# Kernel tuning notes

Measured on AMD Instinct MI355X. Metric: run time of the kernel, lower is better.

## Reference

```python
import jax, jax.numpy as jnp
import numpy as np

N_NODES = 50000
N_EDGES = 800000
N_INC = 64
E_OUTC = 64
HS1 = 128
HS2 = 128
LN_EPS = 1e-5


def setup_inputs() -> dict:
    key = jax.random.key(0)
    ks = jax.random.split(key, 8)
    scale1 = 1.0 / np.sqrt(N_INC + E_OUTC)
    scale2 = 1.0 / np.sqrt(HS1)
    return {
        "x": jax.random.normal(ks[0], (N_NODES, N_INC), dtype=jnp.float32),
        "edge_attr": jax.random.normal(ks[1], (N_EDGES, E_OUTC), dtype=jnp.float32),
        "edge_index": jax.random.randint(ks[2], (2, N_EDGES), 0, N_NODES, dtype=jnp.int64)
        if jax.config.jax_enable_x64 else jax.random.randint(ks[2], (2, N_EDGES), 0, N_NODES, dtype=jnp.int32),
        "W1": jax.random.normal(ks[3], (N_INC + E_OUTC, HS1), dtype=jnp.float32) * scale1,
        "b1": jnp.zeros((HS1,), dtype=jnp.float32),
        "ln_g": jnp.ones((HS1,), dtype=jnp.float32),
        "ln_b": jnp.zeros((HS1,), dtype=jnp.float32),
        "W2": jax.random.normal(ks[4], (HS1, HS2), dtype=jnp.float32) * scale2,
        "b2": jnp.zeros((HS2,), dtype=jnp.float32),
    }


def reference(x, edge_attr, edge_index, W1, b1, ln_g, ln_b, W2, b2):
    # _agg: gather source nodes, concat with edge features -> [E, n_inc+e_outc]
    row, col = edge_index[0], edge_index[1]
    h = jnp.concatenate([x[row], edge_attr], axis=1)
    # node_mlp_1: Linear -> LayerNorm -> ReLU -> Linear
    h = h @ W1 + b1
    mu = jnp.mean(h, axis=-1, keepdims=True)
    var = jnp.mean(jnp.square(h - mu), axis=-1, keepdims=True)
    h = (h - mu) * jax.lax.rsqrt(var + LN_EPS) * ln_g + ln_b
    h = jax.nn.relu(h)
    h = h @ W2 + b2  # [E, HS2]
    # scatter_mean into destination nodes, dim_size = N
    n = x.shape[0]
    sums = jax.ops.segment_sum(h, col, num_segments=n)
    cnt = jax.ops.segment_sum(jnp.ones((h.shape[0],), dtype=h.dtype), col, num_segments=n)
    return sums / jnp.maximum(cnt, 1.0)[:, None]
```

## Files before the change

### kernel.cpp

```cpp
#include <hip/hip_runtime.h>
#include <hip/hip_bf16.h>


typedef __bf16 bf16x8 __attribute__((ext_vector_type(8)));
typedef float f32x4 __attribute__((ext_vector_type(4)));

#define LN_EPS 1e-5f

__device__ __forceinline__ unsigned short bfbits(float f) {
  return __builtin_bit_cast(unsigned short, (__bf16)f);
}
__device__ __forceinline__ float bflo(unsigned int u) { return __uint_as_float(u << 16); }
__device__ __forceinline__ float bfhi(unsigned int u) { return __uint_as_float(u & 0xffff0000u); }
__device__ __forceinline__ unsigned int pkbf(float a, float b) {
  return (unsigned int)bfbits(a) | ((unsigned int)bfbits(b) << 16);
}

__global__ void hist_kernel(const int* __restrict__ eidx, int* __restrict__ cnt, int E) {
  int e = blockIdx.x * blockDim.x + threadIdx.x;
  if (e < E) atomicAdd(&cnt[eidx[E + e]], 1);
}

__global__ void scan_kernel(const int* __restrict__ cnt, int* __restrict__ off, int n) {
  __shared__ int wsum[16];
  __shared__ int carry_s;
  const int tid = threadIdx.x;
  const int wv = tid >> 6;
  const int ln = tid & 63;
  if (tid == 0) carry_s = 0;
  __syncthreads();
  for (int base = 0; base < n; base += 4096) {
    int i0 = base + tid * 4;
    int a = (i0 < n) ? cnt[i0] : 0;
    int b = (i0 + 1 < n) ? cnt[i0 + 1] : 0;
    int c = (i0 + 2 < n) ? cnt[i0 + 2] : 0;
    int d = (i0 + 3 < n) ? cnt[i0 + 3] : 0;
    int lsum = a + b + c + d;
    int sc = lsum;
#pragma unroll
    for (int dl = 1; dl < 64; dl <<= 1) {
      int t = __shfl_up(sc, dl);
      if (ln >= dl) sc += t;
    }
    if (ln == 63) wsum[wv] = sc;
    __syncthreads();
    int woff = 0;
#pragma unroll
    for (int w = 0; w < 16; ++w) {
      int t = wsum[w];
      if (w < wv) woff += t;
    }
    int excl = carry_s + woff + sc - lsum;
    if (i0 < n) off[i0] = excl;
    if (i0 + 1 < n) off[i0 + 1] = excl + a;
    if (i0 + 2 < n) off[i0 + 2] = excl + a + b;
    if (i0 + 3 < n) off[i0 + 3] = excl + a + b + c;
    __syncthreads();
    if (tid == 1023) carry_s = carry_s + woff + sc;
    __syncthreads();
  }
}

__global__ void scatter_kernel(const int* __restrict__ eidx, const int* __restrict__ off,
                               int* __restrict__ cur, int* __restrict__ perm,
                               int* __restrict__ rowp, int E) {
  int e = blockIdx.x * blockDim.x + threadIdx.x;
  if (e < E) {
    int c = eidx[E + e];
    int p = atomicAdd(&cur[c], 1);
    int pos = off[c] + p;
    perm[pos] = e;
    if (rowp) rowp[pos] = eidx[e];
  }
}

template <bool ATOMIC>
__global__ __launch_bounds__(512, 2) void mlp_kernel(
    const float* __restrict__ x, const float* __restrict__ ea,
    const int* __restrict__ eidx, const int* __restrict__ perm,
    const int* __restrict__ rowp, const float* __restrict__ W1,
    const float* __restrict__ b1, const float* __restrict__ lng,
    const float* __restrict__ lnb, const float* __restrict__ W2,
    const float* __restrict__ b2, float* __restrict__ out,
    unsigned short* __restrict__ h2, int E, int ntiles) {
  __shared__ __align__(16) unsigned int w1L[2048 * 4];
  __shared__ __align__(16) unsigned int w2L[2048 * 4];
  __shared__ float b1L[128];
  __shared__ float b2L[128];
  __shared__ unsigned int glcL[128];
  __shared__ __align__(16) char hbuf[8][16 * 272];

  const int tid = threadIdx.x;
  const int lane = tid & 63;
  const int wv = tid >> 6;
  const int e15 = lane & 15;
  const int q = lane >> 4;
  char* hb = hbuf[wv];

  for (int c = tid; c < 2048; c += 512) {
    const int fragid = c >> 6;
    const int l = c & 63;
    const int ks = fragid >> 3, mt = fragid & 7;
    const int qq = l >> 4, ee = l & 15;
    const size_t base = (size_t)(ks * 32 + qq * 8) * 128 + mt * 16 + ee;
    unsigned int p1[4], p2[4];
#pragma unroll
    for (int jj = 0; jj < 4; ++jj) {
      p1[jj] = pkbf(W1[base + (size_t)(2 * jj) * 128], W1[base + (size_t)(2 * jj + 1) * 128]);
      p2[jj] = pkbf(W2[base + (size_t)(2 * jj) * 128], W2[base + (size_t)(2 * jj + 1) * 128]);
    }
    uint4 v1 = {p1[0], p1[1], p1[2], p1[3]};
    uint4 v2 = {p2[0], p2[1], p2[2], p2[3]};
    *(uint4*)&w1L[c * 4] = v1;
    *(uint4*)&w2L[c * 4] = v2;
  }
  if (tid < 128) {
    b1L[tid] = b1[tid];
    b2L[tid] = b2[tid];
    glcL[tid] = pkbf(lng[tid], lnb[tid]);
  }
  __syncthreads();

  const int nwav = (gridDim.x * blockDim.x) >> 6;
  const int wid = (blockIdx.x * blockDim.x + tid) >> 6;

  auto mlp_core = [&](const float4 (&raw)[8], f32x4 (&c2)[8]) {
    bf16x8 bfr[4];
#pragma unroll
    for (int ks = 0; ks < 4; ++ks) {
      const float* p0 = (const float*)&raw[2 * ks];
      const float* p1 = (const float*)&raw[2 * ks + 1];
#pragma unroll
      for (int j = 0; j < 4; ++j) {
        bfr[ks][j] = (__bf16)p0[j];
        bfr[ks][4 + j] = (__bf16)p1[j];
      }
    }
    f32x4 c1[8];
#pragma unroll
    for (int mt = 0; mt < 8; ++mt) {
      float4 bv = *(const float4*)&b1L[mt * 16 + q * 4];
      c1[mt][0] = bv.x;
      c1[mt][1] = bv.y;
      c1[mt][2] = bv.z;
      c1[mt][3] = bv.w;
    }
#pragma unroll
    for (int ks = 0; ks < 4; ++ks)
#pragma unroll
      for (int mt = 0; mt < 8; ++mt) {
        bf16x8 wf = __builtin_bit_cast(
            bf16x8, *(const uint4*)&w1L[((ks * 8 + mt) * 64 + lane) * 4]);
        c1[mt] = __builtin_amdgcn_mfma_f32_16x16x32_bf16(wf, bfr[ks], c1[mt], 0, 0, 0);
      }

    float s = 0.f, ss = 0.f;
#pragma unroll
    for (int mt = 0; mt < 8; ++mt)
#pragma unroll
      for (int r = 0; r < 4; ++r) {
        float v = c1[mt][r];
        s += v;
        ss += v * v;
      }
    s += __shfl_xor(s, 16);
    s += __shfl_xor(s, 32);
    ss += __shfl_xor(ss, 16);
    ss += __shfl_xor(ss, 32);
    const float mu = s * 0.0078125f;
    const float var = ss * 0.0078125f - mu * mu;
    const float inv = rsqrtf(var + LN_EPS);
#pragma unroll
    for (int mt = 0; mt < 8; ++mt) {
      uint4 gv = *(const uint4*)&glcL[mt * 16 + q * 4];
      unsigned int g[4] = {gv.x, gv.y, gv.z, gv.w};
      unsigned short u[4];
#pragma unroll
      for (int r = 0; r < 4; ++r) {
        float v = (c1[mt][r] - mu) * inv;
        v = v * bflo(g[r]) + bfhi(g[r]);
        v = fmaxf(v, 0.f);
        u[r] = bfbits(v);
      }
      uint2 w;
      w.x = (unsigned int)u[0] | ((unsigned int)u[1] << 16);
      w.y = (unsigned int)u[2] | ((unsigned int)u[3] << 16);
      *(uint2*)(hb + e15 * 272 + mt * 32 + q * 8) = w;
    }
    bf16x8 hf[4];
#pragma unroll
    for (int ks = 0; ks < 4; ++ks)
      hf[ks] = __builtin_bit_cast(bf16x8, *(const uint4*)(hb + e15 * 272 + ks * 64 + q * 16));
#pragma unroll
    for (int mt = 0; mt < 8; ++mt) {
      float4 bv = *(const float4*)&b2L[mt * 16 + q * 4];
      c2[mt][0] = bv.x;
      c2[mt][1] = bv.y;
      c2[mt][2] = bv.z;
      c2[mt][3] = bv.w;
    }
#pragma unroll
    for (int ks = 0; ks < 4; ++ks)
#pragma unroll
      for (int mt = 0; mt < 8; ++mt) {
        bf16x8 wf = __builtin_bit_cast(
            bf16x8, *(const uint4*)&w2L[((ks * 8 + mt) * 64 + lane) * 4]);
        c2[mt] = __builtin_amdgcn_mfma_f32_16x16x32_bf16(wf, hf[ks], c2[mt], 0, 0, 0);
      }
  };

  auto store_h2 = [&](int t, const f32x4 (&c2)[8]) {
#pragma unroll
    for (int mt = 0; mt < 8; ++mt) {
      unsigned short u[4];
#pragma unroll
      for (int r = 0; r < 4; ++r) u[r] = bfbits(c2[mt][r]);
      uint2 w;
      w.x = (unsigned int)u[0] | ((unsigned int)u[1] << 16);
      w.y = (unsigned int)u[2] | ((unsigned int)u[3] << 16);
      *(uint2*)(hb + e15 * 272 + mt * 32 + q * 8) = w;
    }
    const int r0 = lane >> 2, c0 = lane & 3;
#pragma unroll
    for (int i = 0; i < 4; ++i) {
      uint4 v = *(const uint4*)(hb + r0 * 272 + (c0 + 4 * i) * 16);
      *(uint4*)((char*)h2 + (size_t)(t * 16 + r0) * 256 + (c0 + 4 * i) * 16) = v;
    }
  };

#define LOADRAW(dst, rowv, ev)                              \
  do {                                                      \
    const float* xr_ = x + (size_t)(rowv)*64;               \
    const float* ar_ = ea + (size_t)(ev)*64;                \
    dst[0] = *(const float4*)(xr_ + q * 8);                 \
    dst[1] = *(const float4*)(xr_ + q * 8 + 4);             \
    dst[2] = *(const float4*)(xr_ + 32 + q * 8);            \
    dst[3] = *(const float4*)(xr_ + 32 + q * 8 + 4);        \
    dst[4] = *(const float4*)(ar_ + q * 8);                 \
    dst[5] = *(const float4*)(ar_ + q * 8 + 4);             \
    dst[6] = *(const float4*)(ar_ + 32 + q * 8);            \
    dst[7] = *(const float4*)(ar_ + 32 + q * 8 + 4);        \
  } while (0)

  if constexpr (!ATOMIC) {
    int tA = wid;
    if (tA >= ntiles) return;
    int pA = tA * 16 + e15;
    int eA = perm[pA];
    int rowA = rowp ? rowp[pA] : eidx[eA];
    int tB = tA + nwav;
    int tBc = (tB < ntiles) ? tB : tA;
    int pB = tBc * 16 + e15;
    int eB = perm[pB];
    int rowB = rowp ? rowp[pB] : eidx[eB];
    float4 rawA[8], rawB[8];
    LOADRAW(rawA, rowA, eA);

    for (int tb = tA; tb < ntiles; tb += 2 * nwav) {
      {
        int tn = tb + 2 * nwav;
        int tc = (tn < ntiles) ? tn : tb;
        int pn = tc * 16 + e15;
        int eAn = perm[pn];
        int rAn = rowp ? rowp[pn] : eidx[eAn];
        LOADRAW(rawB, rowB, eB);
        f32x4 c2[8];
        mlp_core(rawA, c2);
        store_h2(tb, c2);
        eA = eAn;
        rowA = rAn;
      }
      {
        int tcur = tb + nwav;
        int tn = tb + 3 * nwav;
        int tc = (tn < ntiles) ? tn : tb;
        int pn = tc * 16 + e15;
        int eBn = perm[pn];
        int rBn = rowp ? rowp[pn] : eidx[eBn];
        LOADRAW(rawA, rowA, eA);
        if (tcur < ntiles) {
          f32x4 c2[8];
          mlp_core(rawB, c2);
          store_h2(tcur, c2);
        }
        eB = eBn;
        rowB = rBn;
      }
    }
  } else {
    for (int t = wid; t < ntiles; t += nwav) {
      const int pos = t * 16 + e15;
      const int e = pos;
      const int row = eidx[e];
      const int cl = eidx[E + e];
      float4 raw[8];
      LOADRAW(raw, row, e);
      f32x4 c2[8];
      mlp_core(raw, c2);
      float* op = out + (size_t)cl * 128 + q * 4;
#pragma unroll
      for (int mt = 0; mt < 8; ++mt)
#pragma unroll
        for (int r = 0; r < 4; ++r) unsafeAtomicAdd(op + mt * 16 + r, c2[mt][r]);
    }
  }
#undef LOADRAW
}

__global__ void reduce_kernel(const unsigned short* __restrict__ h2,
                              const int* __restrict__ off, const int* __restrict__ cnt,
                              float* __restrict__ out, int N) {
  int tid = blockIdx.x * blockDim.x + threadIdx.x;
  int node = tid >> 4;
  if (node >= N) return;
  int sub = tid & 15;
  int deg = cnt[node];
  int start = off[node];
  float acc[8] = {0.f, 0.f, 0.f, 0.f, 0.f, 0.f, 0.f, 0.f};
  const unsigned short* hp = h2 + (size_t)start * 128 + sub * 8;
  for (int j = 0; j < deg; ++j) {
    uint4 v = *(const uint4*)(hp + (size_t)j * 128);
    acc[0] += bflo(v.x);
    acc[1] += bfhi(v.x);
    acc[2] += bflo(v.y);
    acc[3] += bfhi(v.y);
    acc[4] += bflo(v.z);
    acc[5] += bfhi(v.z);
    acc[6] += bflo(v.w);
    acc[7] += bfhi(v.w);
  }
  float sc = 1.f / (float)(deg > 0 ? deg : 1);
  float* op = out + (size_t)node * 128 + sub * 8;
  float4 o;
  o.x = acc[0] * sc;
  o.y = acc[1] * sc;
  o.z = acc[2] * sc;
  o.w = acc[3] * sc;
  *(float4*)op = o;
  o.x = acc[4] * sc;
  o.y = acc[5] * sc;
  o.z = acc[6] * sc;
  o.w = acc[7] * sc;
  *(float4*)(op + 4) = o;
}

__global__ void divide_kernel(float* __restrict__ out, const int* __restrict__ cnt, int N) {
  int i = blockIdx.x * blockDim.x + threadIdx.x;
  if (i >= N * 32) return;
  int node = i >> 5;
  float s = 1.f / (float)(cnt[node] > 0 ? cnt[node] : 1);
  float4* p = (float4*)out + i;
  float4 v = *p;
  v.x *= s;
  v.y *= s;
  v.z *= s;
  v.w *= s;
  *p = v;
}

extern "C" void kernel_launch(void* const* d_in, const int* in_sizes, int n_in,
                              void* d_out, int out_size, void* d_ws, size_t ws_size,
                              hipStream_t stream) {
  const float* x = (const float*)d_in[0];
  const float* ea = (const float*)d_in[1];
  const int* eidx = (const int*)d_in[2];
  const float* W1 = (const float*)d_in[3];
  const float* b1 = (const float*)d_in[4];
  const float* lng = (const float*)d_in[5];
  const float* lnb = (const float*)d_in[6];
  const float* W2 = (const float*)d_in[7];
  const float* b2 = (const float*)d_in[8];
  float* out = (float*)d_out;

  const int N = in_sizes[0] / 64;
  const int E = in_sizes[1] / 64;
  const int ntiles = E / 16;
  const size_t h2B = (size_t)E * 256;
  const size_t permB = (size_t)E * 4;
  const size_t cB = (size_t)N * 4;
  const size_t need_base = h2B + permB + 3 * cB;
  const size_t need_full = h2B + 2 * permB + 3 * cB;
  const int eblocks = (E + 255) / 256;

  if (ws_size >= need_base) {
    unsigned short* h2 = (unsigned short*)d_ws;
    char* base = (char*)d_ws + h2B;
    int* perm = (int*)base;
    const bool has_rowp = ws_size >= need_full;
    int* rowp = has_rowp ? (int*)(base + permB) : nullptr;
    char* rest = base + (has_rowp ? 2 * permB : permB);
    int* cnt = (int*)rest;
    int* cur = (int*)(rest + cB);
    int* off = (int*)(rest + 2 * cB);
    hipMemsetAsync(cnt, 0, 2 * cB, stream);
    hist_kernel<<<eblocks, 256, 0, stream>>>(eidx, cnt, E);
    scan_kernel<<<1, 1024, 0, stream>>>(cnt, off, N);
    scatter_kernel<<<eblocks, 256, 0, stream>>>(eidx, off, cur, perm, rowp, E);
    mlp_kernel<false><<<256, 512, 0, stream>>>(x, ea, eidx, perm, rowp, W1, b1, lng,
                                               lnb, W2, b2, out, h2, E, ntiles);
    reduce_kernel<<<(N * 16 + 255) / 256, 256, 0, stream>>>(h2, off, cnt, out, N);
  } else {
    int* cnt = (int*)d_ws;
    hipMemsetAsync(out, 0, (size_t)out_size * 4, stream);
    hipMemsetAsync(cnt, 0, cB, stream);
    hist_kernel<<<eblocks, 256, 0, stream>>>(eidx, cnt, E);
    mlp_kernel<true><<<256, 512, 0, stream>>>(x, ea, eidx, nullptr, nullptr, W1, b1,
                                              lng, lnb, W2, b2, out,
                                              (unsigned short*)d_ws, E, ntiles);
    divide_kernel<<<(N * 32 + 255) / 256, 256, 0, stream>>>(out, cnt, N);
  }
}
```

Measured before the change: 548.9 us.

## Fuse segment reduction into MLP kernel with per-tile run-length atomics

```diff
diff --git a/kernel.cpp b/kernel.cpp
--- a/kernel.cpp
+++ b/kernel.cpp
@@ -70,7 +70,7 @@
     int p = atomicAdd(&cur[c], 1);
     int pos = off[c] + p;
     perm[pos] = e;
-    if (rowp) rowp[pos] = eidx[e];
+    rowp[pos] = eidx[e];
   }
 }
 
@@ -78,11 +78,11 @@
 __global__ __launch_bounds__(512, 2) void mlp_kernel(
     const float* __restrict__ x, const float* __restrict__ ea,
     const int* __restrict__ eidx, const int* __restrict__ perm,
-    const int* __restrict__ rowp, const float* __restrict__ W1,
-    const float* __restrict__ b1, const float* __restrict__ lng,
-    const float* __restrict__ lnb, const float* __restrict__ W2,
-    const float* __restrict__ b2, float* __restrict__ out,
-    unsigned short* __restrict__ h2, int E, int ntiles) {
+    const int* __restrict__ rowp, const int* __restrict__ cnt,
+    const float* __restrict__ W1, const float* __restrict__ b1,
+    const float* __restrict__ lng, const float* __restrict__ lnb,
+    const float* __restrict__ W2, const float* __restrict__ b2,
+    float* __restrict__ out, int E, int ntiles) {
   __shared__ __align__(16) unsigned int w1L[2048 * 4];
   __shared__ __align__(16) unsigned int w2L[2048 * 4];
   __shared__ float b1L[128];
@@ -209,7 +209,7 @@
       }
   };
 
-  auto store_h2 = [&](int t, const f32x4 (&c2)[8]) {
+  auto reduce_store = [&](const f32x4 (&c2)[8], int nd, float inv) {
 #pragma unroll
     for (int mt = 0; mt < 8; ++mt) {
       unsigned short u[4];
@@ -220,12 +220,27 @@
       w.y = (unsigned int)u[2] | ((unsigned int)u[3] << 16);
       *(uint2*)(hb + e15 * 272 + mt * 32 + q * 8) = w;
     }
-    const int r0 = lane >> 2, c0 = lane & 3;
-#pragma unroll
-    for (int i = 0; i < 4; ++i) {
-      uint4 v = *(const uint4*)(hb + r0 * 272 + (c0 + 4 * i) * 16);
-      *(uint4*)((char*)h2 + (size_t)(t * 16 + r0) * 256 + (c0 + 4 * i) * 16) = v;
-    }
+    float acc0 = 0.f, acc1 = 0.f;
+    int curn = __shfl(nd, 0);
+    float cinv = __shfl(inv, 0);
+#pragma unroll
+    for (int i = 0; i < 16; ++i) {
+      int ni = __shfl(nd, i);
+      float ii = __shfl(inv, i);
+      if (ni != curn) {
+        unsafeAtomicAdd(out + (size_t)curn * 128 + lane * 2, acc0 * cinv);
+        unsafeAtomicAdd(out + (size_t)curn * 128 + lane * 2 + 1, acc1 * cinv);
+        acc0 = 0.f;
+        acc1 = 0.f;
+        curn = ni;
+        cinv = ii;
+      }
+      unsigned int v = *(const unsigned int*)(hb + i * 272 + lane * 4);
+      acc0 += bflo(v);
+      acc1 += bfhi(v);
+    }
+    unsafeAtomicAdd(out + (size_t)curn * 128 + lane * 2, acc0 * cinv);
+    unsafeAtomicAdd(out + (size_t)curn * 128 + lane * 2 + 1, acc1 * cinv);
   };
 
 #define LOADRAW(dst, rowv, ev)                              \
@@ -247,12 +262,16 @@
     if (tA >= ntiles) return;
     int pA = tA * 16 + e15;
     int eA = perm[pA];
-    int rowA = rowp ? rowp[pA] : eidx[eA];
+    int rowA = rowp[pA];
+    int ndA = eidx[E + eA];
+    float invA = 1.f / (float)cnt[ndA];
     int tB = tA + nwav;
     int tBc = (tB < ntiles) ? tB : tA;
     int pB = tBc * 16 + e15;
     int eB = perm[pB];
-    int rowB = rowp ? rowp[pB] : eidx[eB];
+    int rowB = rowp[pB];
+    int ndB = eidx[E + eB];
+    float invB = 1.f / (float)cnt[ndB];
     float4 rawA[8], rawB[8];
     LOADRAW(rawA, rowA, eA);
 
@@ -262,13 +281,17 @@
         int tc = (tn < ntiles) ? tn : tb;
         int pn = tc * 16 + e15;
         int eAn = perm[pn];
-        int rAn = rowp ? rowp[pn] : eidx[eAn];
+        int rAn = rowp[pn];
+        int nAn = eidx[E + eAn];
+        float iAn = 1.f / (float)cnt[nAn];
         LOADRAW(rawB, rowB, eB);
         f32x4 c2[8];
         mlp_core(rawA, c2);
-        store_h2(tb, c2);
+        reduce_store(c2, ndA, invA);
         eA = eAn;
         rowA = rAn;
+        ndA = nAn;
+        invA = iAn;
       }
       {
         int tcur = tb + nwav;
@@ -276,15 +299,19 @@
         int tc = (tn < ntiles) ? tn : tb;
         int pn = tc * 16 + e15;
         int eBn = perm[pn];
-        int rBn = rowp ? rowp[pn] : eidx[eBn];
+        int rBn = rowp[pn];
+        int nBn = eidx[E + eBn];
+        float iBn = 1.f / (float)cnt[nBn];
         LOADRAW(rawA, rowA, eA);
         if (tcur < ntiles) {
           f32x4 c2[8];
           mlp_core(rawB, c2);
-          store_h2(tcur, c2);
+          reduce_store(c2, ndB, invB);
         }
         eB = eBn;
         rowB = rBn;
+        ndB = nBn;
+        invB = iBn;
       }
     }
   } else {
@@ -305,43 +332,6 @@
     }
   }
 #undef LOADRAW
-}
-
-__global__ void reduce_kernel(const unsigned short* __restrict__ h2,
-                              const int* __restrict__ off, const int* __restrict__ cnt,
-                              float* __restrict__ out, int N) {
-  int tid = blockIdx.x * blockDim.x + threadIdx.x;
-  int node = tid >> 4;
-  if (node >= N) return;
-  int sub = tid & 15;
-  int deg = cnt[node];
-  int start = off[node];
-  float acc[8] = {0.f, 0.f, 0.f, 0.f, 0.f, 0.f, 0.f, 0.f};
-  const unsigned short* hp = h2 + (size_t)start * 128 + sub * 8;
-  for (int j = 0; j < deg; ++j) {
-    uint4 v = *(const uint4*)(hp + (size_t)j * 128);
-    acc[0] += bflo(v.x);
-    acc[1] += bfhi(v.x);
-    acc[2] += bflo(v.y);
-    acc[3] += bfhi(v.y);
-    acc[4] += bflo(v.z);
-    acc[5] += bfhi(v.z);
-    acc[6] += bflo(v.w);
-    acc[7] += bfhi(v.w);
-  }
-  float sc = 1.f / (float)(deg > 0 ? deg : 1);
-  float* op = out + (size_t)node * 128 + sub * 8;
-  float4 o;
-  o.x = acc[0] * sc;
-  o.y = acc[1] * sc;
-  o.z = acc[2] * sc;
-  o.w = acc[3] * sc;
-  *(float4*)op = o;
-  o.x = acc[4] * sc;
-  o.y = acc[5] * sc;
-  o.z = acc[6] * sc;
-  o.w = acc[7] * sc;
-  *(float4*)(op + 4) = o;
 }
 
 __global__ void divide_kernel(float* __restrict__ out, const int* __restrict__ cnt, int N) {
@@ -375,38 +365,31 @@
   const int N = in_sizes[0] / 64;
   const int E = in_sizes[1] / 64;
   const int ntiles = E / 16;
-  const size_t h2B = (size_t)E * 256;
   const size_t permB = (size_t)E * 4;
   const size_t cB = (size_t)N * 4;
-  const size_t need_base = h2B + permB + 3 * cB;
-  const size_t need_full = h2B + 2 * permB + 3 * cB;
+  const size_t need = 2 * permB + 3 * cB;
   const int eblocks = (E + 255) / 256;
 
-  if (ws_size >= need_base) {
-    unsigned short* h2 = (unsigned short*)d_ws;
-    char* base = (char*)d_ws + h2B;
-    int* perm = (int*)base;
-    const bool has_rowp = ws_size >= need_full;
-    int* rowp = has_rowp ? (int*)(base + permB) : nullptr;
-    char* rest = base + (has_rowp ? 2 * permB : permB);
-    int* cnt = (int*)rest;
-    int* cur = (int*)(rest + cB);
-    int* off = (int*)(rest + 2 * cB);
+  if (ws_size >= need) {
+    int* perm = (int*)d_ws;
+    int* rowp = perm + E;
+    int* cnt = rowp + E;
+    int* cur = cnt + N;
+    int* off = cur + N;
+    hipMemsetAsync(out, 0, (size_t)out_size * 4, stream);
     hipMemsetAsync(cnt, 0, 2 * cB, stream);
     hist_kernel<<<eblocks, 256, 0, stream>>>(eidx, cnt, E);
     scan_kernel<<<1, 1024, 0, stream>>>(cnt, off, N);
     scatter_kernel<<<eblocks, 256, 0, stream>>>(eidx, off, cur, perm, rowp, E);
-    mlp_kernel<false><<<256, 512, 0, stream>>>(x, ea, eidx, perm, rowp, W1, b1, lng,
-                                               lnb, W2, b2, out, h2, E, ntiles);
-    reduce_kernel<<<(N * 16 + 255) / 256, 256, 0, stream>>>(h2, off, cnt, out, N);
+    mlp_kernel<false><<<256, 512, 0, stream>>>(x, ea, eidx, perm, rowp, cnt, W1, b1,
+                                               lng, lnb, W2, b2, out, E, ntiles);
   } else {
     int* cnt = (int*)d_ws;
     hipMemsetAsync(out, 0, (size_t)out_size * 4, stream);
     hipMemsetAsync(cnt, 0, cB, stream);
     hist_kernel<<<eblocks, 256, 0, stream>>>(eidx, cnt, E);
-    mlp_kernel<true><<<256, 512, 0, stream>>>(x, ea, eidx, nullptr, nullptr, W1, b1,
-                                              lng, lnb, W2, b2, out,
-                                              (unsigned short*)d_ws, E, ntiles);
+    mlp_kernel<true><<<256, 512, 0, stream>>>(x, ea, eidx, nullptr, nullptr, cnt, W1,
+                                              b1, lng, lnb, W2, b2, out, E, ntiles);
     divide_kernel<<<(N * 32 + 255) / 256, 256, 0, stream>>>(out, cnt, N);
   }
 }
```

After: 489.2 us. -10.9%, faster.
